# Kernel tuning notes

Measured on AMD Instinct MI355X. Metric: run time of the kernel, lower is better.

Reference implementation:

```python
import jax, jax.numpy as jnp
import numpy as np

BINS = 100
MIN, MAX = 0.0, 1.0
DELTA = (MAX - MIN) / BINS
NORM = True
K = 2  # half-window: relu(delta - 0.5*(|dx|+|dy|)) is zero unless |x-c| < 2*delta per axis,
       # and centers are spaced delta apart, so only offsets -2..2 around the containing bin contribute.
BIG = 1e9  # sentinel distance for out-of-range bins -> zero weight


def setup_inputs() -> dict:
    key = jax.random.key(0)
    x = jax.random.uniform(key, (16, 131072, 2), dtype=jnp.float32)  # [B, N, 2] in [0,1)
    return {"x": x}


def reference(x):
    # Faithful to the torch double loop:
    #   counts[b,i,j] = sum_n relu(delta - 0.5*(|x[b,n,0]-c_i| + |x[b,n,1]-c_j|))
    # The triangular kernel has compact support, so each point touches at most a
    # 5x5 neighborhood of bins; compute those weights and scatter-add them.
    B, N, _ = x.shape
    centers = MIN + DELTA * (jnp.arange(BINS, dtype=x.dtype) + 0.5)  # [BINS]
    offs = jnp.arange(-K, K + 1)                                     # [5]

    idx = jnp.floor((x - MIN) / DELTA).astype(jnp.int32)             # [B,N,2] containing bin
    idx = jnp.clip(idx, 0, BINS - 1)
    nb = idx[..., None] + offs                                       # [B,N,2,5] candidate bins
    valid = (nb >= 0) & (nb < BINS)
    nbc = jnp.clip(nb, 0, BINS - 1)

    d = jnp.abs(x[..., None] - centers[nbc])                         # [B,N,2,5] per-axis L1 dist
    d = jnp.where(valid, d, BIG)                                     # kill out-of-range bins

    # combined 5x5 triangular weights per point
    w = jax.nn.relu(DELTA - 0.5 * (d[:, :, 0, :, None] + d[:, :, 1, None, :]))  # [B,N,5,5]

    ii = nbc[:, :, 0, :, None]                                       # [B,N,5,1]
    jj = nbc[:, :, 1, None, :]                                       # [B,N,1,5]
    flat = (jnp.arange(B, dtype=jnp.int32)[:, None, None, None] * (BINS * BINS)
            + ii * BINS + jj)                                        # [B,N,5,5]

    counts = jnp.zeros(B * BINS * BINS, dtype=x.dtype)
    counts = counts.at[flat.reshape(-1)].add(w.reshape(-1))
    counts = counts.reshape(B, BINS, BINS)

    if NORM:
        counts = counts / (counts.sum(axis=(1, 2), keepdims=True) + 1e-5)
    return counts
```

## Files before the change

kernel.cpp:

```cpp
#include <hip/hip_runtime.h>


#define BINS     100
#define NBINS2   (BINS * BINS)
#define NQUAD    (NBINS2 / 4)
#define NPOINTS  131072
#define NBATCH   16
#define PPB      32
#define CHUNK    (NPOINTS / PPB)
#define THREADS  1024
#define NPART    (NBATCH * PPB)
#define QSCALE   33554432.0f
#define QINV     (1.0 / 33554432.0)

__device__ __forceinline__ void accum_point_q(unsigned* lh, float x0, float x1) {
    int i0 = __float2int_rd(__fmul_rn(x0, 100.0f)); i0 = min(max(i0, 0), BINS - 1);
    int i1 = __float2int_rd(__fmul_rn(x1, 100.0f)); i1 = min(max(i1, 0), BINS - 1);
    const float fi0 = (float)i0, fi1 = (float)i1;
    const float c00 = __fmul_rn(0.01f, fi0 + 0.5f);
    const float c10 = __fmul_rn(0.01f, fi1 + 0.5f);
    const float e00 = fabsf(__fsub_rn(x0, c00));
    const float e10 = fabsf(__fsub_rn(x1, c10));
    float e0m = fabsf(__fsub_rn(x0, __fmul_rn(0.01f, fi0 - 0.5f)));
    float e0p = fabsf(__fsub_rn(x0, __fmul_rn(0.01f, fi0 + 1.5f)));
    e0m = (i0 > 0)        ? e0m : 1e9f;
    e0p = (i0 < BINS - 1) ? e0p : 1e9f;
    float e1m = fabsf(__fsub_rn(x1, __fmul_rn(0.01f, fi1 - 0.5f)));
    float e1p = fabsf(__fsub_rn(x1, __fmul_rn(0.01f, fi1 + 1.5f)));
    e1m = (i1 > 0)        ? e1m : 1e9f;
    e1p = (i1 < BINS - 1) ? e1p : 1e9f;
    const bool up0 = (x0 > c00), up1 = (x1 > c10);
    const int   f0  = up0 ? i0 + 2 : i0 - 2;
    const int   f1  = up1 ? i1 + 2 : i1 - 2;
    const float ff0 = up0 ? fi0 + 2.0f : fi0 - 2.0f;
    const float ff1 = up1 ? fi1 + 2.0f : fi1 - 2.0f;
    float e0f = fabsf(__fsub_rn(x0, __fmul_rn(0.01f, ff0 + 0.5f)));
    float e1f = fabsf(__fsub_rn(x1, __fmul_rn(0.01f, ff1 + 0.5f)));
    e0f = ((unsigned)f0 < (unsigned)BINS) ? e0f : 1e9f;
    e1f = ((unsigned)f1 < (unsigned)BINS) ? e1f : 1e9f;

    const int rm = max(i0 - 1, 0) * BINS;
    const int r0 = i0 * BINS;
    const int rp = min(i0 + 1, BINS - 1) * BINS;
    const int rf = min(max(f0, 0), BINS - 1) * BINS;
    const int cm = max(i1 - 1, 0);
    const int cc = i1;
    const int cp = min(i1 + 1, BINS - 1);
    const int cf = min(max(f1, 0), BINS - 1);

    const int B1 = min(max((i1 - 1) & ~1, 0), BINS - 4);
    unsigned q[4];
    #pragma unroll
    for (int k = 0; k < 4; ++k) {
        const int col = B1 + k;
        const float c = __fmul_rn(0.01f, (float)col + 0.5f);
        const float d = fabsf(__fsub_rn(x1, c));
        const float w = fmaf(-0.5f, __fadd_rn(e00, d), 0.01f);
        const bool  v = (abs(col - i1) <= 1) && (w > 0.0f);
        q[k] = v ? (unsigned)fmaf(w, QSCALE, 0.5f) : 0u;
    }
    unsigned long long* lp = (unsigned long long*)(&lh[r0 + B1]);
    atomicAdd(lp,     (unsigned long long)q[0] | ((unsigned long long)q[1] << 32));
    atomicAdd(lp + 1, (unsigned long long)q[2] | ((unsigned long long)q[3] << 32));

#define SITEU(EA, EB, ADDR) do {                                               \
        const float w_ = fmaxf(fmaf(-0.5f, __fadd_rn(EA, EB), 0.01f), 0.0f);   \
        atomicAdd(&lh[ADDR], (unsigned)fmaf(w_, QSCALE, 0.5f));                \
    } while (0)
#define SITEQ(EA, EB, ADDR) do {                                               \
        const float w_ = fmaf(-0.5f, __fadd_rn(EA, EB), 0.01f);                \
        if (w_ > 0.0f)                                                         \
            atomicAdd(&lh[ADDR], (unsigned)fmaf(w_, QSCALE, 0.5f));            \
    } while (0)
    SITEQ(e0m, e1m, rm + cm); SITEU(e0m, e10, rm + cc); SITEQ(e0m, e1p, rm + cp);
    SITEQ(e0p, e1m, rp + cm); SITEU(e0p, e10, rp + cc); SITEQ(e0p, e1p, rp + cp);
    SITEQ(e0f, e10, rf + cc);
    SITEQ(e00, e1f, r0 + cf);
#undef SITEU
#undef SITEQ
}

__global__ __launch_bounds__(THREADS) void hist_part_kernel(
    const float* __restrict__ x, unsigned* __restrict__ part,
    unsigned long long* __restrict__ totals)
{
    __shared__ __align__(16) unsigned lh[NBINS2];
    uint4* lh4 = (uint4*)lh;
    for (int i = threadIdx.x; i < NBINS2 / 4; i += THREADS)
        lh4[i] = make_uint4(0u, 0u, 0u, 0u);
    __syncthreads();

    const int b  = blockIdx.x / PPB;
    const int pb = blockIdx.x % PPB;
    const float4* __restrict__ xp = reinterpret_cast<const float4*>(
        x + (size_t)b * (NPOINTS * 2) + (size_t)pb * (CHUNK * 2));

    #pragma unroll
    for (int k = 0; k < (CHUNK / 2) / THREADS; ++k) {
        const float4 p = xp[threadIdx.x + k * THREADS];
        accum_point_q(lh, p.x, p.y);
        accum_point_q(lh, p.z, p.w);
    }
    __syncthreads();

    uint4* __restrict__ po4 = (uint4*)(part + (size_t)blockIdx.x * NBINS2);
    unsigned long long ts = 0ull;
    for (int i = threadIdx.x; i < NBINS2 / 4; i += THREADS) {
        const uint4 v = lh4[i];
        po4[i] = v;
        ts += (unsigned long long)v.x + v.y + v.z + v.w;
    }
    #pragma unroll
    for (int off = 32; off > 0; off >>= 1) ts += __shfl_down(ts, off, 64);
    if ((threadIdx.x & 63) == 0) atomicAdd(&totals[b], ts);
}

__global__ __launch_bounds__(256) void reduce_norm_kernel(
    const uint4* __restrict__ part4, const unsigned long long* __restrict__ totals,
    float4* __restrict__ out4)
{
    const int b    = blockIdx.x / 10;
    const int ch   = blockIdx.x % 10;
    const int quad = ch * 256 + threadIdx.x;
    if (quad < NQUAD) {
        const uint4* __restrict__ pp = part4 + (size_t)b * PPB * NQUAD + quad;
        unsigned long long s0 = 0, s1 = 0, s2 = 0, s3 = 0;
        #pragma unroll
        for (int p = 0; p < PPB; ++p) {
            const uint4 v = pp[(size_t)p * NQUAD];
            s0 += v.x; s1 += v.y; s2 += v.z; s3 += v.w;
        }
        const double fac = QINV / ((double)totals[b] * QINV + 1e-5);
        out4[(size_t)b * NQUAD + quad] = make_float4(
            (float)((double)s0 * fac), (float)((double)s1 * fac),
            (float)((double)s2 * fac), (float)((double)s3 * fac));
    }
}

__device__ __forceinline__ void accum_point_f(float* lh, float x0, float x1) {
    int i0 = __float2int_rd(__fmul_rn(x0, 100.0f)); i0 = min(max(i0, 0), BINS - 1);
    int i1 = __float2int_rd(__fmul_rn(x1, 100.0f)); i1 = min(max(i1, 0), BINS - 1);
    const float fi0 = (float)i0, fi1 = (float)i1;
    const float c00 = __fmul_rn(0.01f, fi0 + 0.5f);
    const float c10 = __fmul_rn(0.01f, fi1 + 0.5f);
    const float e00 = fabsf(__fsub_rn(x0, c00));
    const float e10 = fabsf(__fsub_rn(x1, c10));
    float e0m = fabsf(__fsub_rn(x0, __fmul_rn(0.01f, fi0 - 0.5f)));
    float e0p = fabsf(__fsub_rn(x0, __fmul_rn(0.01f, fi0 + 1.5f)));
    float e1m = fabsf(__fsub_rn(x1, __fmul_rn(0.01f, fi1 - 0.5f)));
    float e1p = fabsf(__fsub_rn(x1, __fmul_rn(0.01f, fi1 + 1.5f)));
    e0m = (i0 > 0)        ? e0m : 1e9f;
    e0p = (i0 < BINS - 1) ? e0p : 1e9f;
    e1m = (i1 > 0)        ? e1m : 1e9f;
    e1p = (i1 < BINS - 1) ? e1p : 1e9f;
    const bool up0 = (x0 > c00), up1 = (x1 > c10);
    const int   f0  = up0 ? i0 + 2 : i0 - 2;
    const int   f1  = up1 ? i1 + 2 : i1 - 2;
    const float ff0 = up0 ? fi0 + 2.0f : fi0 - 2.0f;
    const float ff1 = up1 ? fi1 + 2.0f : fi1 - 2.0f;
    float e0f = fabsf(__fsub_rn(x0, __fmul_rn(0.01f, ff0 + 0.5f)));
    float e1f = fabsf(__fsub_rn(x1, __fmul_rn(0.01f, ff1 + 0.5f)));
    e0f = ((unsigned)f0 < (unsigned)BINS) ? e0f : 1e9f;
    e1f = ((unsigned)f1 < (unsigned)BINS) ? e1f : 1e9f;
    const int rm = max(i0 - 1, 0) * BINS;
    const int r0 = i0 * BINS;
    const int rp = min(i0 + 1, BINS - 1) * BINS;
    const int rf = min(max(f0, 0), BINS - 1) * BINS;
    const int cm = max(i1 - 1, 0);
    const int cc = i1;
    const int cp = min(i1 + 1, BINS - 1);
    const int cf = min(max(f1, 0), BINS - 1);
#define SITEF(EA, EB, ADDR) do {                                               \
        const float w_ = fmaf(-0.5f, __fadd_rn(EA, EB), 0.01f);                \
        if (w_ > 0.0f) unsafeAtomicAdd(&lh[ADDR], w_);                         \
    } while (0)
    SITEF(e0m, e1m, rm + cm); SITEF(e0m, e10, rm + cc); SITEF(e0m, e1p, rm + cp);
    SITEF(e00, e1m, r0 + cm); SITEF(e00, e10, r0 + cc); SITEF(e00, e1p, r0 + cp);
    SITEF(e0p, e1m, rp + cm); SITEF(e0p, e10, rp + cc); SITEF(e0p, e1p, rp + cp);
    SITEF(e0f, e10, rf + cc);
    SITEF(e00, e1f, r0 + cf);
#undef SITEF
}

__global__ __launch_bounds__(THREADS) void hist_accum_kernel(
    const float* __restrict__ x, float* __restrict__ out)
{
    __shared__ __align__(16) float lh[NBINS2];
    float4* lh4 = (float4*)lh;
    for (int i = threadIdx.x; i < NBINS2 / 4; i += THREADS)
        lh4[i] = make_float4(0.f, 0.f, 0.f, 0.f);
    __syncthreads();
    const int b  = blockIdx.x / PPB;
    const int pb = blockIdx.x % PPB;
    const float4* __restrict__ xp = reinterpret_cast<const float4*>(
        x + (size_t)b * (NPOINTS * 2) + (size_t)pb * (CHUNK * 2));
    #pragma unroll
    for (int k = 0; k < (CHUNK / 2) / THREADS; ++k) {
        const float4 p = xp[threadIdx.x + k * THREADS];
        accum_point_f(lh, p.x, p.y);
        accum_point_f(lh, p.z, p.w);
    }
    __syncthreads();
    float* __restrict__ ob = out + (size_t)b * NBINS2;
    for (int i = threadIdx.x; i < NBINS2; i += THREADS) {
        const float v = lh[i];
        if (v != 0.0f) unsafeAtomicAdd(&ob[i], v);
    }
}

__global__ __launch_bounds__(1024) void norm_kernel(float* __restrict__ out)
{
    const int b = blockIdx.x;
    float* __restrict__ h = out + (size_t)b * NBINS2;
    float local = 0.0f;
    for (int i = threadIdx.x; i < NBINS2; i += 1024) local += h[i];
    #pragma unroll
    for (int off = 32; off > 0; off >>= 1) local += __shfl_down(local, off, 64);
    __shared__ float wsum[16];
    __shared__ float sden;
    if ((threadIdx.x & 63) == 0) wsum[threadIdx.x >> 6] = local;
    __syncthreads();
    if (threadIdx.x == 0) {
        float tt = 0.f;
        #pragma unroll
        for (int i = 0; i < 16; ++i) tt += wsum[i];
        sden = __fadd_rn(tt, 1e-5f);
    }
    __syncthreads();
    const float den = sden;
    for (int i = threadIdx.x; i < NBINS2; i += 1024) h[i] = __fdiv_rn(h[i], den);
}

extern "C" void kernel_launch(void* const* d_in, const int* in_sizes, int n_in,
                              void* d_out, int out_size, void* d_ws, size_t ws_size,
                              hipStream_t stream) {
    (void)in_sizes; (void)n_in;
    const float* x = (const float*)d_in[0];
    float* out = (float*)d_out;

    const size_t need = 128 + (size_t)NPART * NBINS2 * sizeof(unsigned);
    if (ws_size >= need) {
        unsigned long long* totals = (unsigned long long*)d_ws;
        unsigned* part = (unsigned*)((char*)d_ws + 128);
        hipMemsetAsync(totals, 0, NBATCH * sizeof(unsigned long long), stream);
        hist_part_kernel<<<NPART, THREADS, 0, stream>>>(x, part, totals);
        reduce_norm_kernel<<<NBATCH * 10, 256, 0, stream>>>(
            (const uint4*)part, totals, (float4*)out);
    } else {
        hipMemsetAsync(out, 0, (size_t)out_size * sizeof(float), stream);
        hist_accum_kernel<<<NPART, THREADS, 0, stream>>>(x, out);
        norm_kernel<<<NBATCH, 1024, 0, stream>>>(out);
    }
}
```

Baseline: 155.8 us.

## Split histogram sites between shared-memory and global atomics per block

Each point's five cross-shaped neighbor sites are now accumulated with LDS atomics, and the six diagonal and far sites go straight to the block's global partial histogram with global atomics. The final flush does per-bin atomic adds of the LDS histogram into global memory, skipping zero bins, where it previously used vectorized stores. The aim is to cut LDS atomic contention by moving part of the atomic traffic off LDS. In exchange, the whole partial workspace (about 20 MB) must be memset each call, and many scattered global atomics are added, which may cost more than they save.

New measurement: 348.5 us. 124% more time.

```diff
diff --git a/kernel.cpp b/kernel.cpp
--- a/kernel.cpp
+++ b/kernel.cpp
@@ -13,7 +13,9 @@
 #define QSCALE   33554432.0f
 #define QINV     (1.0 / 33554432.0)
 
-__device__ __forceinline__ void accum_point_q(unsigned* lh, float x0, float x1) {
+__device__ __forceinline__ unsigned accum_point_split(
+    unsigned* lh, unsigned* __restrict__ gp, float x0, float x1)
+{
     int i0 = __float2int_rd(__fmul_rn(x0, 100.0f)); i0 = min(max(i0, 0), BINS - 1);
     int i1 = __float2int_rd(__fmul_rn(x1, 100.0f)); i1 = min(max(i1, 0), BINS - 1);
     const float fi0 = (float)i0, fi1 = (float)i1;
@@ -23,10 +25,10 @@
     const float e10 = fabsf(__fsub_rn(x1, c10));
     float e0m = fabsf(__fsub_rn(x0, __fmul_rn(0.01f, fi0 - 0.5f)));
     float e0p = fabsf(__fsub_rn(x0, __fmul_rn(0.01f, fi0 + 1.5f)));
+    float e1m = fabsf(__fsub_rn(x1, __fmul_rn(0.01f, fi1 - 0.5f)));
+    float e1p = fabsf(__fsub_rn(x1, __fmul_rn(0.01f, fi1 + 1.5f)));
     e0m = (i0 > 0)        ? e0m : 1e9f;
     e0p = (i0 < BINS - 1) ? e0p : 1e9f;
-    float e1m = fabsf(__fsub_rn(x1, __fmul_rn(0.01f, fi1 - 0.5f)));
-    float e1p = fabsf(__fsub_rn(x1, __fmul_rn(0.01f, fi1 + 1.5f)));
     e1m = (i1 > 0)        ? e1m : 1e9f;
     e1p = (i1 < BINS - 1) ? e1p : 1e9f;
     const bool up0 = (x0 > c00), up1 = (x1 > c10);
@@ -48,36 +50,33 @@
     const int cp = min(i1 + 1, BINS - 1);
     const int cf = min(max(f1, 0), BINS - 1);
 
-    const int B1 = min(max((i1 - 1) & ~1, 0), BINS - 4);
-    unsigned q[4];
-    #pragma unroll
-    for (int k = 0; k < 4; ++k) {
-        const int col = B1 + k;
-        const float c = __fmul_rn(0.01f, (float)col + 0.5f);
-        const float d = fabsf(__fsub_rn(x1, c));
-        const float w = fmaf(-0.5f, __fadd_rn(e00, d), 0.01f);
-        const bool  v = (abs(col - i1) <= 1) && (w > 0.0f);
-        q[k] = v ? (unsigned)fmaf(w, QSCALE, 0.5f) : 0u;
-    }
-    unsigned long long* lp = (unsigned long long*)(&lh[r0 + B1]);
-    atomicAdd(lp,     (unsigned long long)q[0] | ((unsigned long long)q[1] << 32));
-    atomicAdd(lp + 1, (unsigned long long)q[2] | ((unsigned long long)q[3] << 32));
-
-#define SITEU(EA, EB, ADDR) do {                                               \
-        const float w_ = fmaxf(fmaf(-0.5f, __fadd_rn(EA, EB), 0.01f), 0.0f);   \
-        atomicAdd(&lh[ADDR], (unsigned)fmaf(w_, QSCALE, 0.5f));                \
-    } while (0)
-#define SITEQ(EA, EB, ADDR) do {                                               \
+#define SITEL(EA, EB, ADDR) do {                                               \
         const float w_ = fmaf(-0.5f, __fadd_rn(EA, EB), 0.01f);                \
         if (w_ > 0.0f)                                                         \
             atomicAdd(&lh[ADDR], (unsigned)fmaf(w_, QSCALE, 0.5f));            \
     } while (0)
-    SITEQ(e0m, e1m, rm + cm); SITEU(e0m, e10, rm + cc); SITEQ(e0m, e1p, rm + cp);
-    SITEQ(e0p, e1m, rp + cm); SITEU(e0p, e10, rp + cc); SITEQ(e0p, e1p, rp + cp);
-    SITEQ(e0f, e10, rf + cc);
-    SITEQ(e00, e1f, r0 + cf);
-#undef SITEU
-#undef SITEQ
+    SITEL(e0m, e10, rm + cc);
+    SITEL(e00, e1m, r0 + cm);
+    SITEL(e00, e10, r0 + cc);
+    SITEL(e00, e1p, r0 + cp);
+    SITEL(e0p, e10, rp + cc);
+#undef SITEL
+
+    unsigned off = 0u;
+#define SITEG(EA, EB, ADDR) do {                                               \
+        const float w_ = fmaf(-0.5f, __fadd_rn(EA, EB), 0.01f);                \
+        if (w_ > 0.0f) {                                                       \
+            const unsigned q_ = (unsigned)fmaf(w_, QSCALE, 0.5f);              \
+            atomicAdd(&gp[ADDR], q_);                                          \
+            off += q_;                                                         \
+        }                                                                      \
+    } while (0)
+    SITEG(e0m, e1m, rm + cm); SITEG(e0m, e1p, rm + cp);
+    SITEG(e0p, e1m, rp + cm); SITEG(e0p, e1p, rp + cp);
+    SITEG(e0f, e10, rf + cc);
+    SITEG(e00, e1f, r0 + cf);
+#undef SITEG
+    return off;
 }
 
 __global__ __launch_bounds__(THREADS) void hist_part_kernel(
@@ -92,23 +91,24 @@
 
     const int b  = blockIdx.x / PPB;
     const int pb = blockIdx.x % PPB;
+    unsigned* __restrict__ gp = part + (size_t)blockIdx.x * NBINS2;
     const float4* __restrict__ xp = reinterpret_cast<const float4*>(
         x + (size_t)b * (NPOINTS * 2) + (size_t)pb * (CHUNK * 2));
 
+    unsigned offsum = 0u;
     #pragma unroll
     for (int k = 0; k < (CHUNK / 2) / THREADS; ++k) {
         const float4 p = xp[threadIdx.x + k * THREADS];
-        accum_point_q(lh, p.x, p.y);
-        accum_point_q(lh, p.z, p.w);
-    }
-    __syncthreads();
-
-    uint4* __restrict__ po4 = (uint4*)(part + (size_t)blockIdx.x * NBINS2);
-    unsigned long long ts = 0ull;
-    for (int i = threadIdx.x; i < NBINS2 / 4; i += THREADS) {
-        const uint4 v = lh4[i];
-        po4[i] = v;
-        ts += (unsigned long long)v.x + v.y + v.z + v.w;
+        offsum += accum_point_split(lh, gp, p.x, p.y);
+        offsum += accum_point_split(lh, gp, p.z, p.w);
+    }
+    __syncthreads();
+
+    unsigned long long ts = (unsigned long long)offsum;
+    for (int i = threadIdx.x; i < NBINS2; i += THREADS) {
+        const unsigned v = lh[i];
+        if (v) atomicAdd(&gp[i], v);
+        ts += v;
     }
     #pragma unroll
     for (int off = 32; off > 0; off >>= 1) ts += __shfl_down(ts, off, 64);
@@ -242,7 +242,7 @@
     if (ws_size >= need) {
         unsigned long long* totals = (unsigned long long*)d_ws;
         unsigned* part = (unsigned*)((char*)d_ws + 128);
-        hipMemsetAsync(totals, 0, NBATCH * sizeof(unsigned long long), stream);
+        hipMemsetAsync(d_ws, 0, need, stream);
         hist_part_kernel<<<NPART, THREADS, 0, stream>>>(x, part, totals);
         reduce_norm_kernel<<<NBATCH * 10, 256, 0, stream>>>(
             (const uint4*)part, totals, (float4*)out);
```
